# Optimization experiments

Hardware: AMD Instinct MI355X
Metric: run time of the kernel (lower is better)

The kernel has to match this reference:

```python
import jax, jax.numpy as jnp
import numpy as np

N, E, G = 50000, 800000, 64
IN, H, C = 128, 3, 64
HC = H * C


def _conv(x, src, dst, Wq, bq, Wk, bk, Wv, bv, Ws, bs, Wb):
    # node-level projections, then per-edge gather
    q = (x @ Wq + bq).reshape(-1, H, C)[dst]   # [E,H,C]
    k = (x @ Wk + bk).reshape(-1, H, C)[src]
    v = (x @ Wv + bv).reshape(-1, H, C)[src]
    alpha = (q * k).sum(-1) / jnp.sqrt(jnp.float32(C))  # [E,H]
    # segment softmax over incoming edges of each target node
    amax = jax.ops.segment_max(alpha, dst, num_segments=N)
    amax = jnp.where(jnp.isfinite(amax), amax, 0.0)
    ex = jnp.exp(alpha - amax[dst])
    denom = jax.ops.segment_sum(ex, dst, num_segments=N)
    a = ex / (denom[dst] + 1e-16)
    out = jax.ops.segment_sum(a[:, :, None] * v, dst, num_segments=N).reshape(-1, HC)
    # gated skip (beta=True, root_weight=True)
    r = x @ Ws + bs
    beta = jax.nn.sigmoid(jnp.concatenate([out, r, out - r], -1) @ Wb)  # [N,1]
    return beta * r + (1.0 - beta) * out


def setup_inputs() -> dict:
    key = jax.random.key(0)
    ks = jax.random.split(key, 32)
    x = jax.random.normal(ks[0], (N, IN), dtype=jnp.float32)
    edge_index = jax.random.randint(ks[1], (2, E), 0, N, dtype=jnp.int32)
    batch = jnp.sort(jax.random.randint(ks[2], (N,), 0, G, dtype=jnp.int32))
    s = 0.05
    def w(k, shape):
        return jax.random.normal(k, shape, dtype=jnp.float32) * s
    d = {"x": x, "edge_index": edge_index, "batch": batch}
    ins = [IN, HC]
    ki = 3
    for l in range(2):
        din = ins[l]
        d[f"Wq{l}"] = w(ks[ki], (din, HC)); ki += 1
        d[f"bq{l}"] = jnp.zeros((HC,), jnp.float32)
        d[f"Wk{l}"] = w(ks[ki], (din, HC)); ki += 1
        d[f"bk{l}"] = jnp.zeros((HC,), jnp.float32)
        d[f"Wv{l}"] = w(ks[ki], (din, HC)); ki += 1
        d[f"bv{l}"] = jnp.zeros((HC,), jnp.float32)
        d[f"Ws{l}"] = w(ks[ki], (din, HC)); ki += 1
        d[f"bs{l}"] = jnp.zeros((HC,), jnp.float32)
        d[f"Wb{l}"] = w(ks[ki], (3 * HC, 1)); ki += 1
    d["Wlin"] = w(ks[ki], (HC, 1)); ki += 1
    d["blin"] = jnp.zeros((1,), jnp.float32)
    return d


def reference(x, edge_index, batch,
              Wq0, bq0, Wk0, bk0, Wv0, bv0, Ws0, bs0, Wb0,
              Wq1, bq1, Wk1, bk1, Wv1, bv1, Ws1, bs1, Wb1,
              Wlin, blin):
    src, dst = edge_index[0], edge_index[1]
    h = _conv(x, src, dst, Wq0, bq0, Wk0, bk0, Wv0, bv0, Ws0, bs0, Wb0)
    h = jax.nn.elu(h)
    h = _conv(h, src, dst, Wq1, bq1, Wk1, bk1, Wv1, bv1, Ws1, bs1, Wb1)
    h = jax.nn.elu(h)
    # global mean pool over graphs
    cnt = jax.ops.segment_sum(jnp.ones((N,), jnp.float32), batch, num_segments=G)
    pooled = jax.ops.segment_sum(h, batch, num_segments=G) / jnp.maximum(cnt, 1.0)[:, None]
    logits = (pooled @ Wlin + blin).squeeze(-1)  # [G]
    return logits
```

## Files before the change

### kernel.cpp

```cpp
#include <hip/hip_runtime.h>
#include <math.h>

#define NNODES 50000
#define NEDGES 800000
#define NGRAPH 64
#define DIM_IN 128
#define HCDIM  192
#define QKVRW  768

typedef __attribute__((ext_vector_type(8))) short short8;
typedef __attribute__((ext_vector_type(4))) float f32x4;
typedef __attribute__((ext_vector_type(2))) float f32x2;

__device__ __forceinline__ unsigned short f2bf(float f){
  unsigned int u = __float_as_uint(f);
  unsigned int r = (u + 0x7fffu + ((u>>16)&1u)) >> 16;
  return (unsigned short)r;
}

__device__ __forceinline__ float4 bf4_to_f4(uint2 u){
  float4 f;
  f.x = __uint_as_float(u.x<<16);
  f.y = __uint_as_float(u.x & 0xffff0000u);
  f.z = __uint_as_float(u.y<<16);
  f.w = __uint_as_float(u.y & 0xffff0000u);
  return f;
}

__device__ __forceinline__ float4 fp8x4_to_f4(unsigned int u){
  f32x2 lo = __builtin_amdgcn_cvt_pk_f32_fp8((int)u, false);
  f32x2 hi = __builtin_amdgcn_cvt_pk_f32_fp8((int)u, true);
  float4 f; f.x=lo[0]; f.y=lo[1]; f.z=hi[0]; f.w=hi[1];
  return f;
}

__device__ __forceinline__ float wave_sum(float v){
#pragma unroll
  for(int off=32; off>0; off>>=1) v += __shfl_xor(v, off, 64);
  return v;
}

__global__ void zero2_k(int* a, int* b, int n){
  int i = blockIdx.x*blockDim.x + threadIdx.x;
  if(i<n){ a[i]=0; b[i]=0; }
}

__global__ void hist_k(const int* __restrict__ dst, int* __restrict__ counts, int E){
  int e = blockIdx.x*blockDim.x + threadIdx.x;
  if(e<E) atomicAdd(&counts[dst[e]], 1);
}

__global__ void scan_partial(const int* __restrict__ counts, int* __restrict__ bsum, int N){
  __shared__ int lds[256];
  int t = threadIdx.x;
  int idx = blockIdx.x*256 + t;
  int v = (idx<N)? counts[idx] : 0;
  lds[t]=v; __syncthreads();
#pragma unroll
  for(int off=128; off>0; off>>=1){
    if(t<off) lds[t]+=lds[t+off];
    __syncthreads();
  }
  if(t==0) bsum[blockIdx.x]=lds[0];
}

__global__ void scan_bsum(int* bsum, int nb){
  __shared__ int lds[1024];
  int t=threadIdx.x;
  int v=(t<nb)?bsum[t]:0;
  lds[t]=v; __syncthreads();
  int x=v;
#pragma unroll
  for(int off=1; off<1024; off<<=1){
    int y=(t>=off)?lds[t-off]:0;
    __syncthreads();
    x+=y; lds[t]=x;
    __syncthreads();
  }
  if(t<nb) bsum[t]=x-v;
}

__global__ void scan_final(const int* __restrict__ counts, const int* __restrict__ bsum,
                           int* __restrict__ row_ptr, int N){
  __shared__ int lds[256];
  int t=threadIdx.x;
  int idx=blockIdx.x*256+t;
  int v=(idx<N)?counts[idx]:0;
  lds[t]=v; __syncthreads();
  int x=v;
#pragma unroll
  for(int off=1; off<256; off<<=1){
    int y=(t>=off)?lds[t-off]:0;
    __syncthreads();
    x+=y; lds[t]=x;
    __syncthreads();
  }
  if(idx<=N) row_ptr[idx]= bsum[blockIdx.x]+x-v;
}

__global__ void fill_k(const int* __restrict__ src, const int* __restrict__ dst,
                       const int* __restrict__ row_ptr, int* __restrict__ cursor,
                       int* __restrict__ csr_src, int E){
  int e = blockIdx.x*blockDim.x + threadIdx.x;
  if(e<E){
    int d = dst[e];
    int pos = row_ptr[d] + atomicAdd(&cursor[d], 1);
    csr_src[pos] = src[e];
  }
}

#define CAST_BLKS (NNODES*DIM_IN/4/256)
__global__ void prep0_k(const float* __restrict__ X, unsigned short* __restrict__ Xb,
                        const float* __restrict__ Wq, const float* __restrict__ Wk,
                        const float* __restrict__ Wv, const float* __restrict__ Ws,
                        const float* __restrict__ bq, const float* __restrict__ bk,
                        const float* __restrict__ bv, const float* __restrict__ bs,
                        unsigned short* __restrict__ Wt, float* __restrict__ bcat){
  if(blockIdx.x < CAST_BLKS){
    int i4 = (blockIdx.x*256 + threadIdx.x)*4;
    float4 v = *(const float4*)(X+i4);
    ushort4 o; o.x=f2bf(v.x); o.y=f2bf(v.y); o.z=f2bf(v.z); o.w=f2bf(v.w);
    *(ushort4*)(Xb+i4) = o;
  } else {
    int idx = (blockIdx.x-CAST_BLKS)*256 + threadIdx.x;
    if(idx < QKVRW*DIM_IN){
      int c = idx / DIM_IN, k = idx % DIM_IN;
      int mat = c/HCDIM, cm = c%HCDIM;
      const float* W = (mat==0)?Wq:(mat==1)?Ws:(mat==2)?Wk:Wv;
      Wt[(size_t)c*DIM_IN + k] = f2bf(W[(size_t)k*HCDIM + cm]);
    }
    if(idx < QKVRW){
      int mat = idx/HCDIM, cm = idx%HCDIM;
      const float* b = (mat==0)?bq:(mat==1)?bs:(mat==2)?bk:bv;
      bcat[idx] = b[cm];
    }
  }
}

__global__ void build_wt(const float* __restrict__ Wq, const float* __restrict__ Wk,
                         const float* __restrict__ Wv, const float* __restrict__ Ws,
                         const float* __restrict__ bq, const float* __restrict__ bk,
                         const float* __restrict__ bv, const float* __restrict__ bs,
                         unsigned short* __restrict__ Wt, float* __restrict__ bcat, int K){
  int idx = blockIdx.x*256 + threadIdx.x;
  if(idx < QKVRW*K){
    int c = idx / K, k = idx % K;
    int mat = c/HCDIM, cm = c%HCDIM;
    const float* W = (mat==0)?Wq:(mat==1)?Ws:(mat==2)?Wk:Wv;
    Wt[(size_t)c*K + k] = f2bf(W[(size_t)k*HCDIM + cm]);
  }
  if(idx < QKVRW){
    int mat = idx/HCDIM, cm = idx%HCDIM;
    const float* b = (mat==0)?bq:(mat==1)?bs:(mat==2)?bk:bv;
    bcat[idx] = b[cm];
  }
}

template<int K>
__global__ __launch_bounds__(256) void gemm_mfma(
    const unsigned short* __restrict__ Xb,
    const unsigned short* __restrict__ Wt,
    const float* __restrict__ bcat,
    unsigned short* __restrict__ QR,
    unsigned char* __restrict__ KV, int N)
{
  __shared__ unsigned short As[128*64];
  __shared__ unsigned short Bs[128*64];
  const int tid = threadIdx.x;
  const int wv = tid>>6;
  const int lane = tid&63;
  const int m0  = blockIdx.x*128;
  const int nc0 = blockIdx.y*128;

  const int wr = wv>>1, wc = wv&1;
  const int lhi = lane>>4, llo = lane&15;
  f32x4 acc[4][4] = {};

  constexpr int NT = K/64;
#pragma unroll
  for(int kt=0; kt<NT; ++kt){
    if(kt>0) __syncthreads();
#pragma unroll
    for(int it=0; it<4; ++it){
      int p = it*256 + tid;
      int r = p>>3, c = p&7;
      int cs = c ^ (r&7);
      int grow = m0 + r; if(grow > N-1) grow = N-1;
      const unsigned short* gp = Xb + (size_t)grow*K + kt*64 + cs*8;
      unsigned short* lp = As + (size_t)(it*256 + wv*64)*8;
      __builtin_amdgcn_global_load_lds(
          (const __attribute__((address_space(1))) unsigned int*)gp,
          (__attribute__((address_space(3))) unsigned int*)lp, 16, 0, 0);
    }
#pragma unroll
    for(int it=0; it<4; ++it){
      int p = it*256 + tid;
      int r = p>>3, c = p&7;
      int cs = c ^ (r&7);
      const unsigned short* gp = Wt + (size_t)(nc0 + r)*K + kt*64 + cs*8;
      unsigned short* lp = Bs + (size_t)(it*256 + wv*64)*8;
      __builtin_amdgcn_global_load_lds(
          (const __attribute__((address_space(1))) unsigned int*)gp,
          (__attribute__((address_space(3))) unsigned int*)lp, 16, 0, 0);
    }
    __syncthreads();

#pragma unroll
    for(int kk=0; kk<64; kk+=32){
      short8 a[4], b[4];
      const int chunk = (kk>>3) + lhi;
#pragma unroll
      for(int i=0;i<4;++i){
        int rr = wr*64 + i*16 + llo;
        int cs = chunk ^ (rr&7);
        a[i] = *(const short8*)(As + rr*64 + cs*8);
      }
#pragma unroll
      for(int j=0;j<4;++j){
        int cc = wc*64 + j*16 + llo;
        int cs = chunk ^ (cc&7);
        b[j] = *(const short8*)(Bs + cc*64 + cs*8);
      }
#pragma unroll
      for(int i=0;i<4;++i)
#pragma unroll
        for(int j=0;j<4;++j)
          acc[i][j] = __builtin_amdgcn_mfma_f32_16x16x32_bf16(a[i], b[j], acc[i][j], 0,0,0);
    }
  }

  if(nc0 < 384){
#pragma unroll
    for(int j=0;j<4;++j){
      const int col = nc0 + wc*64 + j*16 + llo;
      const float bias = bcat[col];
#pragma unroll
      for(int i=0;i<4;++i){
#pragma unroll
        for(int r=0;r<4;++r){
          int grow = m0 + wr*64 + i*16 + lhi*4 + r;
          if(grow < N) QR[(size_t)grow*384 + col] = f2bf(acc[i][j][r] + bias);
        }
      }
    }
  } else {
#pragma unroll
    for(int j=0;j<4;++j){
      const int col = nc0 - 384 + wc*64 + j*16 + llo;
      const float bias = bcat[col + 384];
#pragma unroll
      for(int i=0;i<4;++i){
#pragma unroll
        for(int r=0;r<4;++r){
          int grow = m0 + wr*64 + i*16 + lhi*4 + r;
          float v0 = acc[i][j][r] + bias;
          float n0 = __shfl_xor(v0, 1, 64);
          if(((llo&1)==0) && grow < N){
            int p0 = __builtin_amdgcn_cvt_pk_fp8_f32(v0, n0, 0, false);
            *(unsigned short*)(KV + (size_t)grow*384 + col) = (unsigned short)(p0 & 0xffff);
          }
        }
      }
    }
  }
}

template<bool OUTBF>
__global__ __launch_bounds__(256) void attn_kernel(
  const unsigned short* __restrict__ QR,
  const unsigned char* __restrict__ KV,
  const int* __restrict__ row_ptr, const int* __restrict__ csr_src,
  const float* __restrict__ Wb, float* __restrict__ HoutF,
  unsigned short* __restrict__ HoutB, int N)
{
  const int wave = threadIdx.x>>6;
  const int lane = threadIdx.x&63;
  const int g    = lane>>4;
  const int l    = lane&15;
  const int n = blockIdx.x*4 + wave;
  if(n>=N) return;

  const unsigned short* nr = QR + (size_t)n*384 + 4*l;
  float4 q0 = bf4_to_f4(*(const uint2*)(nr));
  float4 q1 = bf4_to_f4(*(const uint2*)(nr+64));
  float4 q2 = bf4_to_f4(*(const uint2*)(nr+128));

  const int s0 = row_ptr[n];
  const int deg = row_ptr[n+1]-s0;

  float4 a0={0,0,0,0}, a1={0,0,0,0}, a2={0,0,0,0};
  float d0=0.f,d1=0.f,d2=0.f;

  unsigned int ku0=0,ku1=0,ku2=0,vu0=0,vu1=0,vu2=0;
  if(deg>0){
    int i0 = s0 + (g<deg ? g : 0); if(i0 > NEDGES-1) i0 = NEDGES-1;
    int sCur = csr_src[i0];
    const unsigned int* kv = (const unsigned int*)(KV + (size_t)sCur*384) + l;
    ku0=kv[0]; ku1=kv[16]; ku2=kv[32]; vu0=kv[48]; vu1=kv[64]; vu2=kv[80];
  }
  for(int base=0; base<deg; base+=4){
    const int inext = base + 4 + g;
    const int sNxt = csr_src[s0 + (inext<deg ? inext : 0)];
    const unsigned int* kvN = (const unsigned int*)(KV + (size_t)sNxt*384) + l;
    unsigned int nk0=kvN[0], nk1=kvN[16], nk2=kvN[32];
    unsigned int nv0=kvN[48], nv1=kvN[64], nv2=kvN[80];

    const bool valid = (base + g < deg);
    float4 k0 = fp8x4_to_f4(ku0);
    float4 k1 = fp8x4_to_f4(ku1);
    float4 k2 = fp8x4_to_f4(ku2);
    float p0 = q0.x*k0.x+q0.y*k0.y+q0.z*k0.z+q0.w*k0.w;
    float p1 = q1.x*k1.x+q1.y*k1.y+q1.z*k1.z+q1.w*k1.w;
    float p2 = q2.x*k2.x+q2.y*k2.y+q2.z*k2.z+q2.w*k2.w;
#pragma unroll
    for(int off=1; off<16; off<<=1){
      p0 += __shfl_xor(p0, off, 64);
      p1 += __shfl_xor(p1, off, 64);
      p2 += __shfl_xor(p2, off, 64);
    }
    float e0 = valid ? __expf(0.125f*p0) : 0.f;
    float e1 = valid ? __expf(0.125f*p1) : 0.f;
    float e2 = valid ? __expf(0.125f*p2) : 0.f;
    d0 += e0; d1 += e1; d2 += e2;
    float4 v0 = fp8x4_to_f4(vu0);
    float4 v1 = fp8x4_to_f4(vu1);
    float4 v2 = fp8x4_to_f4(vu2);
    a0.x+=e0*v0.x; a0.y+=e0*v0.y; a0.z+=e0*v0.z; a0.w+=e0*v0.w;
    a1.x+=e1*v1.x; a1.y+=e1*v1.y; a1.z+=e1*v1.z; a1.w+=e1*v1.w;
    a2.x+=e2*v2.x; a2.y+=e2*v2.y; a2.z+=e2*v2.z; a2.w+=e2*v2.w;

    ku0=nk0; ku1=nk1; ku2=nk2; vu0=nv0; vu1=nv1; vu2=nv2;
  }

#pragma unroll
  for(int off=16; off<64; off<<=1){
    a0.x+=__shfl_xor(a0.x,off,64); a0.y+=__shfl_xor(a0.y,off,64);
    a0.z+=__shfl_xor(a0.z,off,64); a0.w+=__shfl_xor(a0.w,off,64);
    a1.x+=__shfl_xor(a1.x,off,64); a1.y+=__shfl_xor(a1.y,off,64);
    a1.z+=__shfl_xor(a1.z,off,64); a1.w+=__shfl_xor(a1.w,off,64);
    a2.x+=__shfl_xor(a2.x,off,64); a2.y+=__shfl_xor(a2.y,off,64);
    a2.z+=__shfl_xor(a2.z,off,64); a2.w+=__shfl_xor(a2.w,off,64);
    d0+=__shfl_xor(d0,off,64); d1+=__shfl_xor(d1,off,64); d2+=__shfl_xor(d2,off,64);
  }
  const float id0=1.f/(d0+1e-16f), id1=1.f/(d1+1e-16f), id2=1.f/(d2+1e-16f);
  float4 o0, o1, o2;
  o0.x=a0.x*id0; o0.y=a0.y*id0; o0.z=a0.z*id0; o0.w=a0.w*id0;
  o1.x=a1.x*id1; o1.y=a1.y*id1; o1.z=a1.z*id1; o1.w=a1.w*id1;
  o2.x=a2.x*id2; o2.y=a2.y*id2; o2.z=a2.z*id2; o2.w=a2.w*id2;

  float4 r0 = bf4_to_f4(*(const uint2*)(nr+192));
  float4 r1 = bf4_to_f4(*(const uint2*)(nr+256));
  float4 r2 = bf4_to_f4(*(const uint2*)(nr+320));

  const float* wb = Wb + 4*l;
  float4 w00=*(const float4*)(wb),     w01=*(const float4*)(wb+64),  w02=*(const float4*)(wb+128);
  float4 w10=*(const float4*)(wb+192), w11=*(const float4*)(wb+256), w12=*(const float4*)(wb+320);
  float4 w20=*(const float4*)(wb+384), w21=*(const float4*)(wb+448), w22=*(const float4*)(wb+512);
  float z =
    o0.x*w00.x+o0.y*w00.y+o0.z*w00.z+o0.w*w00.w +
    o1.x*w01.x+o1.y*w01.y+o1.z*w01.z+o1.w*w01.w +
    o2.x*w02.x+o2.y*w02.y+o2.z*w02.z+o2.w*w02.w +
    r0.x*w10.x+r0.y*w10.y+r0.z*w10.z+r0.w*w10.w +
    r1.x*w11.x+r1.y*w11.y+r1.z*w11.z+r1.w*w11.w +
    r2.x*w12.x+r2.y*w12.y+r2.z*w12.z+r2.w*w12.w +
    (o0.x-r0.x)*w20.x+(o0.y-r0.y)*w20.y+(o0.z-r0.z)*w20.z+(o0.w-r0.w)*w20.w +
    (o1.x-r1.x)*w21.x+(o1.y-r1.y)*w21.y+(o1.z-r1.z)*w21.z+(o1.w-r1.w)*w21.w +
    (o2.x-r2.x)*w22.x+(o2.y-r2.y)*w22.y+(o2.z-r2.z)*w22.z+(o2.w-r2.w)*w22.w;
#pragma unroll
  for(int off=1; off<16; off<<=1) z += __shfl_xor(z, off, 64);
  const float beta = 1.f/(1.f+__expf(-z));
  float4 h0,h1,h2;
  h0.x=beta*r0.x+(1.f-beta)*o0.x; h0.y=beta*r0.y+(1.f-beta)*o0.y;
  h0.z=beta*r0.z+(1.f-beta)*o0.z; h0.w=beta*r0.w+(1.f-beta)*o0.w;
  h1.x=beta*r1.x+(1.f-beta)*o1.x; h1.y=beta*r1.y+(1.f-beta)*o1.y;
  h1.z=beta*r1.z+(1.f-beta)*o1.z; h1.w=beta*r1.w+(1.f-beta)*o1.w;
  h2.x=beta*r2.x+(1.f-beta)*o2.x; h2.y=beta*r2.y+(1.f-beta)*o2.y;
  h2.z=beta*r2.z+(1.f-beta)*o2.z; h2.w=beta*r2.w+(1.f-beta)*o2.w;
  h0.x=(h0.x>0.f)?h0.x:expm1f(h0.x); h0.y=(h0.y>0.f)?h0.y:expm1f(h0.y);
  h0.z=(h0.z>0.f)?h0.z:expm1f(h0.z); h0.w=(h0.w>0.f)?h0.w:expm1f(h0.w);
  h1.x=(h1.x>0.f)?h1.x:expm1f(h1.x); h1.y=(h1.y>0.f)?h1.y:expm1f(h1.y);
  h1.z=(h1.z>0.f)?h1.z:expm1f(h1.z); h1.w=(h1.w>0.f)?h1.w:expm1f(h1.w);
  h2.x=(h2.x>0.f)?h2.x:expm1f(h2.x); h2.y=(h2.y>0.f)?h2.y:expm1f(h2.y);
  h2.z=(h2.z>0.f)?h2.z:expm1f(h2.z); h2.w=(h2.w>0.f)?h2.w:expm1f(h2.w);
  if(g==0){
    if(OUTBF){
      unsigned short* hb = HoutB + (size_t)n*HCDIM + 4*l;
      ushort4 u0, u1, u2;
      u0.x=f2bf(h0.x); u0.y=f2bf(h0.y); u0.z=f2bf(h0.z); u0.w=f2bf(h0.w);
      u1.x=f2bf(h1.x); u1.y=f2bf(h1.y); u1.z=f2bf(h1.z); u1.w=f2bf(h1.w);
      u2.x=f2bf(h2.x); u2.y=f2bf(h2.y); u2.z=f2bf(h2.z); u2.w=f2bf(h2.w);
      *(ushort4*)(hb)     = u0;
      *(ushort4*)(hb+64)  = u1;
      *(ushort4*)(hb+128) = u2;
    } else {
      float* ho = HoutF + (size_t)n*HCDIM + 4*l;
      *(float4*)(ho)     = h0;
      *(float4*)(ho+64)  = h1;
      *(float4*)(ho+128) = h2;
    }
  }
}

__global__ void zero_pool(float* pooled, int* cnt){
  int i = blockIdx.x*256 + threadIdx.x;
  if(i < NGRAPH*HCDIM) ((int*)pooled)[i]=0;
  if(i < NGRAPH) cnt[i]=0;
}

__global__ void pool_k(const float* __restrict__ H, const int* __restrict__ batch,
                       float* __restrict__ pooled, int* __restrict__ cnt, int N){
  const int t = threadIdx.x;
  int start = blockIdx.x*256;
  int end = min(start+256, N);
  if(start>=N) return;
  int cur = batch[start];
  float acc = 0.f;
  int run = 0;
  for(int nn=start; nn<end; ++nn){
    int g = batch[nn];
    if(g!=cur){
      atomicAdd(&pooled[(size_t)cur*HCDIM+t], acc);
      if(t==0) atomicAdd(&cnt[cur], run);
      acc=0.f; run=0; cur=g;
    }
    acc += H[(size_t)nn*HCDIM+t];
    run++;
  }
  atomicAdd(&pooled[(size_t)cur*HCDIM+t], acc);
  if(t==0) atomicAdd(&cnt[cur], run);
}

__global__ void logits_k(const float* __restrict__ pooled, const int* __restrict__ cnt,
                         const float* __restrict__ Wlin, const float* __restrict__ blin,
                         float* __restrict__ out){
  const int g = blockIdx.x;
  const int lane = threadIdx.x;
  float c = fmaxf((float)cnt[g], 1.f);
  float s = 0.f;
#pragma unroll
  for(int j=0;j<3;++j){
    int col = j*64+lane;
    s += pooled[(size_t)g*HCDIM+col]/c * Wlin[col];
  }
  s = wave_sum(s);
  if(lane==0) out[g] = s + blin[0];
}

extern "C" void kernel_launch(void* const* d_in, const int* in_sizes, int n_in,
                              void* d_out, int out_size, void* d_ws, size_t ws_size,
                              hipStream_t stream)
{
  const int N=NNODES, E=NEDGES;
  const float* x     = (const float*)d_in[0];
  const int*   ei    = (const int*)d_in[1];
  const int*   batch = (const int*)d_in[2];
  const int* esrc = ei;
  const int* edst = ei + E;
  const float* Wq0=(const float*)d_in[3];  const float* bq0=(const float*)d_in[4];
  const float* Wk0=(const float*)d_in[5];  const float* bk0=(const float*)d_in[6];
  const float* Wv0=(const float*)d_in[7];  const float* bv0=(const float*)d_in[8];
  const float* Ws0=(const float*)d_in[9];  const float* bs0=(const float*)d_in[10];
  const float* Wb0=(const float*)d_in[11];
  const float* Wq1=(const float*)d_in[12]; const float* bq1=(const float*)d_in[13];
  const float* Wk1=(const float*)d_in[14]; const float* bk1=(const float*)d_in[15];
  const float* Wv1=(const float*)d_in[16]; const float* bv1=(const float*)d_in[17];
  const float* Ws1=(const float*)d_in[18]; const float* bs1=(const float*)d_in[19];
  const float* Wb1=(const float*)d_in[20];
  const float* Wlin=(const float*)d_in[21];
  const float* blin=(const float*)d_in[22];
  float* out = (float*)d_out;

  char* p = (char*)d_ws;
  auto alloc = [&](size_t bytes)->char*{
    char* q = p; p += (bytes+255)/256*256; return q;
  };
  unsigned short* Xb   = (unsigned short*)alloc((size_t)N*HCDIM*2);
  unsigned short* QR   = (unsigned short*)alloc((size_t)N*384*2);
  unsigned char*  KV   = (unsigned char*)alloc((size_t)N*384);
  float* H1            = (float*)alloc((size_t)N*HCDIM*4);
  unsigned short* Wt   = (unsigned short*)alloc((size_t)QKVRW*HCDIM*2);
  float* bcat          = (float*)alloc(QKVRW*4);
  int* counts  = (int*)alloc((size_t)N*4);
  int* cursor  = (int*)alloc((size_t)N*4);
  int* row_ptr = (int*)alloc((size_t)(N+1)*4);
  int* csr     = (int*)alloc((size_t)E*4);
  int* bsum    = (int*)alloc(4096);
  float* pooled= (float*)alloc((size_t)NGRAPH*HCDIM*4);
  int* cnt     = (int*)alloc(256);

  const int NB = (N+255)/256;

  zero2_k<<<(N+255)/256,256,0,stream>>>(counts,cursor,N);
  hist_k<<<(E+255)/256,256,0,stream>>>(edst,counts,E);
  scan_partial<<<NB,256,0,stream>>>(counts,bsum,N);
  scan_bsum<<<1,1024,0,stream>>>(bsum,NB);
  scan_final<<<NB,256,0,stream>>>(counts,bsum,row_ptr,N);
  fill_k<<<(E+255)/256,256,0,stream>>>(esrc,edst,row_ptr,cursor,csr,E);

  dim3 ggemm((N+127)/128, 6);
  prep0_k<<<CAST_BLKS + (QKVRW*DIM_IN+255)/256, 256, 0, stream>>>(
      x, Xb, Wq0,Wk0,Wv0,Ws0, bq0,bk0,bv0,bs0, Wt, bcat);
  gemm_mfma<DIM_IN><<<ggemm,256,0,stream>>>(Xb,Wt,bcat,QR,KV,N);
  attn_kernel<true><<<(N+3)/4,256,0,stream>>>(QR,KV,row_ptr,csr,Wb0,nullptr,Xb,N);
  build_wt<<<(QKVRW*HCDIM+255)/256,256,0,stream>>>(Wq1,Wk1,Wv1,Ws1,bq1,bk1,bv1,bs1,Wt,bcat,HCDIM);
  gemm_mfma<HCDIM><<<ggemm,256,0,stream>>>(Xb,Wt,bcat,QR,KV,N);
  attn_kernel<false><<<(N+3)/4,256,0,stream>>>(QR,KV,row_ptr,csr,Wb1,H1,nullptr,N);

  zero_pool<<<(NGRAPH*HCDIM+255)/256,256,0,stream>>>(pooled,cnt);
  pool_k<<<(N+255)/256,192,0,stream>>>(H1,batch,pooled,cnt,N);
  logits_k<<<NGRAPH,64,0,stream>>>(pooled,cnt,Wlin,blin,out);
}
```

Baseline: 408.5 us.

## Merge weight prep kernels, use memsets, and pack attention math into float2 ops

Folds the layer-0 and layer-1 weight transpose/cast into one prep kernel with separate weight buffers. The zeroing kernels are replaced by hipMemsetAsync calls, which cuts the launch count. The attention kernel is rewritten around float2 vectors so the compiler can emit packed FMA, and the 1/sqrt(C) scale is folded into q once instead of applied per edge. Operation order changes slightly, which can shift rounding.

```diff
diff --git a/kernel.cpp b/kernel.cpp
--- a/kernel.cpp
+++ b/kernel.cpp
@@ -18,31 +18,24 @@
   return (unsigned short)r;
 }
 
-__device__ __forceinline__ float4 bf4_to_f4(uint2 u){
-  float4 f;
-  f.x = __uint_as_float(u.x<<16);
-  f.y = __uint_as_float(u.x & 0xffff0000u);
-  f.z = __uint_as_float(u.y<<16);
-  f.w = __uint_as_float(u.y & 0xffff0000u);
-  return f;
-}
-
-__device__ __forceinline__ float4 fp8x4_to_f4(unsigned int u){
-  f32x2 lo = __builtin_amdgcn_cvt_pk_f32_fp8((int)u, false);
-  f32x2 hi = __builtin_amdgcn_cvt_pk_f32_fp8((int)u, true);
-  float4 f; f.x=lo[0]; f.y=lo[1]; f.z=hi[0]; f.w=hi[1];
-  return f;
+__device__ __forceinline__ f32x2 bf2_to_f2(unsigned int u){
+  f32x2 r;
+  r[0] = __uint_as_float(u<<16);
+  r[1] = __uint_as_float(u & 0xffff0000u);
+  return r;
+}
+
+__device__ __forceinline__ f32x2 fp8_lo(unsigned int u){
+  return __builtin_amdgcn_cvt_pk_f32_fp8((int)u, false);
+}
+__device__ __forceinline__ f32x2 fp8_hi(unsigned int u){
+  return __builtin_amdgcn_cvt_pk_f32_fp8((int)u, true);
 }
 
 __device__ __forceinline__ float wave_sum(float v){
 #pragma unroll
   for(int off=32; off>0; off>>=1) v += __shfl_xor(v, off, 64);
   return v;
-}
-
-__global__ void zero2_k(int* a, int* b, int n){
-  int i = blockIdx.x*blockDim.x + threadIdx.x;
-  if(i<n){ a[i]=0; b[i]=0; }
 }
 
 __global__ void hist_k(const int* __restrict__ dst, int* __restrict__ counts, int E){
@@ -110,49 +103,52 @@
 }
 
 #define CAST_BLKS (NNODES*DIM_IN/4/256)
-__global__ void prep0_k(const float* __restrict__ X, unsigned short* __restrict__ Xb,
-                        const float* __restrict__ Wq, const float* __restrict__ Wk,
-                        const float* __restrict__ Wv, const float* __restrict__ Ws,
-                        const float* __restrict__ bq, const float* __restrict__ bk,
-                        const float* __restrict__ bv, const float* __restrict__ bs,
-                        unsigned short* __restrict__ Wt, float* __restrict__ bcat){
-  if(blockIdx.x < CAST_BLKS){
-    int i4 = (blockIdx.x*256 + threadIdx.x)*4;
+#define WT0_BLKS  ((QKVRW*DIM_IN+255)/256)
+#define WT1_BLKS  ((QKVRW*HCDIM+255)/256)
+__global__ void prep_all(const float* __restrict__ X, unsigned short* __restrict__ Xb,
+  const float* __restrict__ Wq0,const float* __restrict__ Wk0,
+  const float* __restrict__ Wv0,const float* __restrict__ Ws0,
+  const float* __restrict__ bq0,const float* __restrict__ bk0,
+  const float* __restrict__ bv0,const float* __restrict__ bs0,
+  unsigned short* __restrict__ Wt0, float* __restrict__ bcat0,
+  const float* __restrict__ Wq1,const float* __restrict__ Wk1,
+  const float* __restrict__ Wv1,const float* __restrict__ Ws1,
+  const float* __restrict__ bq1,const float* __restrict__ bk1,
+  const float* __restrict__ bv1,const float* __restrict__ bs1,
+  unsigned short* __restrict__ Wt1, float* __restrict__ bcat1)
+{
+  const int b = blockIdx.x;
+  if(b < CAST_BLKS){
+    int i4 = (b*256 + threadIdx.x)*4;
     float4 v = *(const float4*)(X+i4);
     ushort4 o; o.x=f2bf(v.x); o.y=f2bf(v.y); o.z=f2bf(v.z); o.w=f2bf(v.w);
     *(ushort4*)(Xb+i4) = o;
-  } else {
-    int idx = (blockIdx.x-CAST_BLKS)*256 + threadIdx.x;
+  } else if(b < CAST_BLKS+WT0_BLKS){
+    int idx = (b-CAST_BLKS)*256 + threadIdx.x;
     if(idx < QKVRW*DIM_IN){
       int c = idx / DIM_IN, k = idx % DIM_IN;
       int mat = c/HCDIM, cm = c%HCDIM;
-      const float* W = (mat==0)?Wq:(mat==1)?Ws:(mat==2)?Wk:Wv;
-      Wt[(size_t)c*DIM_IN + k] = f2bf(W[(size_t)k*HCDIM + cm]);
+      const float* W = (mat==0)?Wq0:(mat==1)?Ws0:(mat==2)?Wk0:Wv0;
+      Wt0[(size_t)c*DIM_IN + k] = f2bf(W[(size_t)k*HCDIM + cm]);
     }
     if(idx < QKVRW){
       int mat = idx/HCDIM, cm = idx%HCDIM;
-      const float* b = (mat==0)?bq:(mat==1)?bs:(mat==2)?bk:bv;
-      bcat[idx] = b[cm];
-    }
-  }
-}
-
-__global__ void build_wt(const float* __restrict__ Wq, const float* __restrict__ Wk,
-                         const float* __restrict__ Wv, const float* __restrict__ Ws,
-                         const float* __restrict__ bq, const float* __restrict__ bk,
-                         const float* __restrict__ bv, const float* __restrict__ bs,
-                         unsigned short* __restrict__ Wt, float* __restrict__ bcat, int K){
-  int idx = blockIdx.x*256 + threadIdx.x;
-  if(idx < QKVRW*K){
-    int c = idx / K, k = idx % K;
-    int mat = c/HCDIM, cm = c%HCDIM;
-    const float* W = (mat==0)?Wq:(mat==1)?Ws:(mat==2)?Wk:Wv;
-    Wt[(size_t)c*K + k] = f2bf(W[(size_t)k*HCDIM + cm]);
-  }
-  if(idx < QKVRW){
-    int mat = idx/HCDIM, cm = idx%HCDIM;
-    const float* b = (mat==0)?bq:(mat==1)?bs:(mat==2)?bk:bv;
-    bcat[idx] = b[cm];
+      const float* bb = (mat==0)?bq0:(mat==1)?bs0:(mat==2)?bk0:bv0;
+      bcat0[idx] = bb[cm];
+    }
+  } else {
+    int idx = (b-CAST_BLKS-WT0_BLKS)*256 + threadIdx.x;
+    if(idx < QKVRW*HCDIM){
+      int c = idx / HCDIM, k = idx % HCDIM;
+      int mat = c/HCDIM, cm = c%HCDIM;
+      const float* W = (mat==0)?Wq1:(mat==1)?Ws1:(mat==2)?Wk1:Wv1;
+      Wt1[(size_t)c*HCDIM + k] = f2bf(W[(size_t)k*HCDIM + cm]);
+    }
+    if(idx < QKVRW){
+      int mat = idx/HCDIM, cm = idx%HCDIM;
+      const float* bb = (mat==0)?bq1:(mat==1)?bs1:(mat==2)?bk1:bv1;
+      bcat1[idx] = bb[cm];
+    }
   }
 }
 
@@ -281,14 +277,19 @@
   if(n>=N) return;
 
   const unsigned short* nr = QR + (size_t)n*384 + 4*l;
-  float4 q0 = bf4_to_f4(*(const uint2*)(nr));
-  float4 q1 = bf4_to_f4(*(const uint2*)(nr+64));
-  float4 q2 = bf4_to_f4(*(const uint2*)(nr+128));
+  f32x2 qlo[3], qhi[3];
+#pragma unroll
+  for(int h=0;h<3;++h){
+    uint2 u = *(const uint2*)(nr + 64*h);
+    qlo[h] = bf2_to_f2(u.x) * 0.125f;
+    qhi[h] = bf2_to_f2(u.y) * 0.125f;
+  }
 
   const int s0 = row_ptr[n];
   const int deg = row_ptr[n+1]-s0;
 
-  float4 a0={0,0,0,0}, a1={0,0,0,0}, a2={0,0,0,0};
+  f32x2 aLo[3] = {{0,0},{0,0},{0,0}};
+  f32x2 aHi[3] = {{0,0},{0,0},{0,0}};
   float d0=0.f,d1=0.f,d2=0.f;
 
   unsigned int ku0=0,ku1=0,ku2=0,vu0=0,vu1=0,vu2=0;
@@ -306,105 +307,92 @@
     unsigned int nv0=kvN[48], nv1=kvN[64], nv2=kvN[80];
 
     const bool valid = (base + g < deg);
-    float4 k0 = fp8x4_to_f4(ku0);
-    float4 k1 = fp8x4_to_f4(ku1);
-    float4 k2 = fp8x4_to_f4(ku2);
-    float p0 = q0.x*k0.x+q0.y*k0.y+q0.z*k0.z+q0.w*k0.w;
-    float p1 = q1.x*k1.x+q1.y*k1.y+q1.z*k1.z+q1.w*k1.w;
-    float p2 = q2.x*k2.x+q2.y*k2.y+q2.z*k2.z+q2.w*k2.w;
+    f32x2 t0 = qlo[0]*fp8_lo(ku0) + qhi[0]*fp8_hi(ku0);
+    f32x2 t1 = qlo[1]*fp8_lo(ku1) + qhi[1]*fp8_hi(ku1);
+    f32x2 t2 = qlo[2]*fp8_lo(ku2) + qhi[2]*fp8_hi(ku2);
+    float p0 = t0[0]+t0[1];
+    float p1 = t1[0]+t1[1];
+    float p2 = t2[0]+t2[1];
 #pragma unroll
     for(int off=1; off<16; off<<=1){
       p0 += __shfl_xor(p0, off, 64);
       p1 += __shfl_xor(p1, off, 64);
       p2 += __shfl_xor(p2, off, 64);
     }
-    float e0 = valid ? __expf(0.125f*p0) : 0.f;
-    float e1 = valid ? __expf(0.125f*p1) : 0.f;
-    float e2 = valid ? __expf(0.125f*p2) : 0.f;
+    float e0 = valid ? __expf(p0) : 0.f;
+    float e1 = valid ? __expf(p1) : 0.f;
+    float e2 = valid ? __expf(p2) : 0.f;
     d0 += e0; d1 += e1; d2 += e2;
-    float4 v0 = fp8x4_to_f4(vu0);
-    float4 v1 = fp8x4_to_f4(vu1);
-    float4 v2 = fp8x4_to_f4(vu2);
-    a0.x+=e0*v0.x; a0.y+=e0*v0.y; a0.z+=e0*v0.z; a0.w+=e0*v0.w;
-    a1.x+=e1*v1.x; a1.y+=e1*v1.y; a1.z+=e1*v1.z; a1.w+=e1*v1.w;
-    a2.x+=e2*v2.x; a2.y+=e2*v2.y; a2.z+=e2*v2.z; a2.w+=e2*v2.w;
+    f32x2 e20 = {e0,e0}, e21 = {e1,e1}, e22 = {e2,e2};
+    aLo[0] = fp8_lo(vu0)*e20 + aLo[0];
+    aHi[0] = fp8_hi(vu0)*e20 + aHi[0];
+    aLo[1] = fp8_lo(vu1)*e21 + aLo[1];
+    aHi[1] = fp8_hi(vu1)*e21 + aHi[1];
+    aLo[2] = fp8_lo(vu2)*e22 + aLo[2];
+    aHi[2] = fp8_hi(vu2)*e22 + aHi[2];
 
     ku0=nk0; ku1=nk1; ku2=nk2; vu0=nv0; vu1=nv1; vu2=nv2;
   }
 
 #pragma unroll
   for(int off=16; off<64; off<<=1){
-    a0.x+=__shfl_xor(a0.x,off,64); a0.y+=__shfl_xor(a0.y,off,64);
-    a0.z+=__shfl_xor(a0.z,off,64); a0.w+=__shfl_xor(a0.w,off,64);
-    a1.x+=__shfl_xor(a1.x,off,64); a1.y+=__shfl_xor(a1.y,off,64);
-    a1.z+=__shfl_xor(a1.z,off,64); a1.w+=__shfl_xor(a1.w,off,64);
-    a2.x+=__shfl_xor(a2.x,off,64); a2.y+=__shfl_xor(a2.y,off,64);
-    a2.z+=__shfl_xor(a2.z,off,64); a2.w+=__shfl_xor(a2.w,off,64);
+#pragma unroll
+    for(int h=0;h<3;++h){
+      aLo[h][0]+=__shfl_xor(aLo[h][0],off,64); aLo[h][1]+=__shfl_xor(aLo[h][1],off,64);
+      aHi[h][0]+=__shfl_xor(aHi[h][0],off,64); aHi[h][1]+=__shfl_xor(aHi[h][1],off,64);
+    }
     d0+=__shfl_xor(d0,off,64); d1+=__shfl_xor(d1,off,64); d2+=__shfl_xor(d2,off,64);
   }
-  const float id0=1.f/(d0+1e-16f), id1=1.f/(d1+1e-16f), id2=1.f/(d2+1e-16f);
-  float4 o0, o1, o2;
-  o0.x=a0.x*id0; o0.y=a0.y*id0; o0.z=a0.z*id0; o0.w=a0.w*id0;
-  o1.x=a1.x*id1; o1.y=a1.y*id1; o1.z=a1.z*id1; o1.w=a1.w*id1;
-  o2.x=a2.x*id2; o2.y=a2.y*id2; o2.z=a2.z*id2; o2.w=a2.w*id2;
-
-  float4 r0 = bf4_to_f4(*(const uint2*)(nr+192));
-  float4 r1 = bf4_to_f4(*(const uint2*)(nr+256));
-  float4 r2 = bf4_to_f4(*(const uint2*)(nr+320));
-
-  const float* wb = Wb + 4*l;
-  float4 w00=*(const float4*)(wb),     w01=*(const float4*)(wb+64),  w02=*(const float4*)(wb+128);
-  float4 w10=*(const float4*)(wb+192), w11=*(const float4*)(wb+256), w12=*(const float4*)(wb+320);
-  float4 w20=*(const float4*)(wb+384), w21=*(const float4*)(wb+448), w22=*(const float4*)(wb+512);
-  float z =
-    o0.x*w00.x+o0.y*w00.y+o0.z*w00.z+o0.w*w00.w +
-    o1.x*w01.x+o1.y*w01.y+o1.z*w01.z+o1.w*w01.w +
-    o2.x*w02.x+o2.y*w02.y+o2.z*w02.z+o2.w*w02.w +
-    r0.x*w10.x+r0.y*w10.y+r0.z*w10.z+r0.w*w10.w +
-    r1.x*w11.x+r1.y*w11.y+r1.z*w11.z+r1.w*w11.w +
-    r2.x*w12.x+r2.y*w12.y+r2.z*w12.z+r2.w*w12.w +
-    (o0.x-r0.x)*w20.x+(o0.y-r0.y)*w20.y+(o0.z-r0.z)*w20.z+(o0.w-r0.w)*w20.w +
-    (o1.x-r1.x)*w21.x+(o1.y-r1.y)*w21.y+(o1.z-r1.z)*w21.z+(o1.w-r1.w)*w21.w +
-    (o2.x-r2.x)*w22.x+(o2.y-r2.y)*w22.y+(o2.z-r2.z)*w22.z+(o2.w-r2.w)*w22.w;
+  const float dsum[3] = {d0,d1,d2};
+  f32x2 oLo[3], oHi[3], rLo[3], rHi[3];
+#pragma unroll
+  for(int h=0;h<3;++h){
+    float inv = 1.f/(dsum[h]+1e-16f);
+    oLo[h] = aLo[h]*inv; oHi[h] = aHi[h]*inv;
+    uint2 ur = *(const uint2*)(nr + 192 + 64*h);
+    rLo[h] = bf2_to_f2(ur.x); rHi[h] = bf2_to_f2(ur.y);
+  }
+
+  f32x2 zz = {0,0};
+#pragma unroll
+  for(int h=0;h<3;++h){
+    const float* wO = Wb + 64*h + 4*l;
+    const float* wR = Wb + 192 + 64*h + 4*l;
+    const float* wD = Wb + 384 + 64*h + 4*l;
+    f32x2 woL = *(const f32x2*)(wO), woH = *(const f32x2*)(wO+2);
+    f32x2 wrL = *(const f32x2*)(wR), wrH = *(const f32x2*)(wR+2);
+    f32x2 wdL = *(const f32x2*)(wD), wdH = *(const f32x2*)(wD+2);
+    zz = oLo[h]*woL + zz;
+    zz = oHi[h]*woH + zz;
+    zz = rLo[h]*wrL + zz;
+    zz = rHi[h]*wrH + zz;
+    zz = (oLo[h]-rLo[h])*wdL + zz;
+    zz = (oHi[h]-rHi[h])*wdH + zz;
+  }
+  float z = zz[0]+zz[1];
 #pragma unroll
   for(int off=1; off<16; off<<=1) z += __shfl_xor(z, off, 64);
   const float beta = 1.f/(1.f+__expf(-z));
-  float4 h0,h1,h2;
-  h0.x=beta*r0.x+(1.f-beta)*o0.x; h0.y=beta*r0.y+(1.f-beta)*o0.y;
-  h0.z=beta*r0.z+(1.f-beta)*o0.z; h0.w=beta*r0.w+(1.f-beta)*o0.w;
-  h1.x=beta*r1.x+(1.f-beta)*o1.x; h1.y=beta*r1.y+(1.f-beta)*o1.y;
-  h1.z=beta*r1.z+(1.f-beta)*o1.z; h1.w=beta*r1.w+(1.f-beta)*o1.w;
-  h2.x=beta*r2.x+(1.f-beta)*o2.x; h2.y=beta*r2.y+(1.f-beta)*o2.y;
-  h2.z=beta*r2.z+(1.f-beta)*o2.z; h2.w=beta*r2.w+(1.f-beta)*o2.w;
-  h0.x=(h0.x>0.f)?h0.x:expm1f(h0.x); h0.y=(h0.y>0.f)?h0.y:expm1f(h0.y);
-  h0.z=(h0.z>0.f)?h0.z:expm1f(h0.z); h0.w=(h0.w>0.f)?h0.w:expm1f(h0.w);
-  h1.x=(h1.x>0.f)?h1.x:expm1f(h1.x); h1.y=(h1.y>0.f)?h1.y:expm1f(h1.y);
-  h1.z=(h1.z>0.f)?h1.z:expm1f(h1.z); h1.w=(h1.w>0.f)?h1.w:expm1f(h1.w);
-  h2.x=(h2.x>0.f)?h2.x:expm1f(h2.x); h2.y=(h2.y>0.f)?h2.y:expm1f(h2.y);
-  h2.z=(h2.z>0.f)?h2.z:expm1f(h2.z); h2.w=(h2.w>0.f)?h2.w:expm1f(h2.w);
+
   if(g==0){
-    if(OUTBF){
-      unsigned short* hb = HoutB + (size_t)n*HCDIM + 4*l;
-      ushort4 u0, u1, u2;
-      u0.x=f2bf(h0.x); u0.y=f2bf(h0.y); u0.z=f2bf(h0.z); u0.w=f2bf(h0.w);
-      u1.x=f2bf(h1.x); u1.y=f2bf(h1.y); u1.z=f2bf(h1.z); u1.w=f2bf(h1.w);
-      u2.x=f2bf(h2.x); u2.y=f2bf(h2.y); u2.z=f2bf(h2.z); u2.w=f2bf(h2.w);
-      *(ushort4*)(hb)     = u0;
-      *(ushort4*)(hb+64)  = u1;
-      *(ushort4*)(hb+128) = u2;
-    } else {
-      float* ho = HoutF + (size_t)n*HCDIM + 4*l;
-      *(float4*)(ho)     = h0;
-      *(float4*)(ho+64)  = h1;
-      *(float4*)(ho+128) = h2;
-    }
-  }
-}
-
-__global__ void zero_pool(float* pooled, int* cnt){
-  int i = blockIdx.x*256 + threadIdx.x;
-  if(i < NGRAPH*HCDIM) ((int*)pooled)[i]=0;
-  if(i < NGRAPH) cnt[i]=0;
+#pragma unroll
+    for(int h=0;h<3;++h){
+      f32x2 hL = (rLo[h]-oLo[h])*beta + oLo[h];
+      f32x2 hH = (rHi[h]-oHi[h])*beta + oHi[h];
+      hL[0]=(hL[0]>0.f)?hL[0]:expm1f(hL[0]); hL[1]=(hL[1]>0.f)?hL[1]:expm1f(hL[1]);
+      hH[0]=(hH[0]>0.f)?hH[0]:expm1f(hH[0]); hH[1]=(hH[1]>0.f)?hH[1]:expm1f(hH[1]);
+      if(OUTBF){
+        unsigned short* hb = HoutB + (size_t)n*HCDIM + 64*h + 4*l;
+        ushort4 u;
+        u.x=f2bf(hL[0]); u.y=f2bf(hL[1]); u.z=f2bf(hH[0]); u.w=f2bf(hH[1]);
+        *(ushort4*)(hb) = u;
+      } else {
+        float* ho = HoutF + (size_t)n*HCDIM + 64*h + 4*l;
+        float4 f; f.x=hL[0]; f.y=hL[1]; f.z=hH[0]; f.w=hH[1];
+        *(float4*)(ho) = f;
+      }
+    }
+  }
 }
 
 __global__ void pool_k(const float* __restrict__ H, const int* __restrict__ batch,
@@ -478,10 +466,13 @@
   unsigned short* QR   = (unsigned short*)alloc((size_t)N*384*2);
   unsigned char*  KV   = (unsigned char*)alloc((size_t)N*384);
   float* H1            = (float*)alloc((size_t)N*HCDIM*4);
-  unsigned short* Wt   = (unsigned short*)alloc((size_t)QKVRW*HCDIM*2);
-  float* bcat          = (float*)alloc(QKVRW*4);
-  int* counts  = (int*)alloc((size_t)N*4);
-  int* cursor  = (int*)alloc((size_t)N*4);
+  unsigned short* Wt0  = (unsigned short*)alloc((size_t)QKVRW*DIM_IN*2);
+  float* bcat0         = (float*)alloc(QKVRW*4);
+  unsigned short* Wt1  = (unsigned short*)alloc((size_t)QKVRW*HCDIM*2);
+  float* bcat1         = (float*)alloc(QKVRW*4);
+  const size_t CSR_CHUNK = ((size_t)N*4+255)/256*256;
+  int* counts  = (int*)alloc(CSR_CHUNK);
+  int* cursor  = (int*)alloc(CSR_CHUNK);
   int* row_ptr = (int*)alloc((size_t)(N+1)*4);
   int* csr     = (int*)alloc((size_t)E*4);
   int* bsum    = (int*)alloc(4096);
@@ -490,7 +481,14 @@
 
   const int NB = (N+255)/256;
 
-  zero2_k<<<(N+255)/256,256,0,stream>>>(counts,cursor,N);
+  hipMemsetAsync(counts, 0, 2*CSR_CHUNK, stream);
+  hipMemsetAsync(pooled, 0, (size_t)NGRAPH*HCDIM*4 + 256, stream);
+
+  prep_all<<<CAST_BLKS + WT0_BLKS + WT1_BLKS, 256, 0, stream>>>(
+      x, Xb,
+      Wq0,Wk0,Wv0,Ws0, bq0,bk0,bv0,bs0, Wt0, bcat0,
+      Wq1,Wk1,Wv1,Ws1, bq1,bk1,bv1,bs1, Wt1, bcat1);
+
   hist_k<<<(E+255)/256,256,0,stream>>>(edst,counts,E);
   scan_partial<<<NB,256,0,stream>>>(counts,bsum,N);
   scan_bsum<<<1,1024,0,stream>>>(bsum,NB);
@@ -498,15 +496,11 @@
   fill_k<<<(E+255)/256,256,0,stream>>>(esrc,edst,row_ptr,cursor,csr,E);
 
   dim3 ggemm((N+127)/128, 6);
-  prep0_k<<<CAST_BLKS + (QKVRW*DIM_IN+255)/256, 256, 0, stream>>>(
-      x, Xb, Wq0,Wk0,Wv0,Ws0, bq0,bk0,bv0,bs0, Wt, bcat);
-  gemm_mfma<DIM_IN><<<ggemm,256,0,stream>>>(Xb,Wt,bcat,QR,KV,N);
+  gemm_mfma<DIM_IN><<<ggemm,256,0,stream>>>(Xb,Wt0,bcat0,QR,KV,N);
   attn_kernel<true><<<(N+3)/4,256,0,stream>>>(QR,KV,row_ptr,csr,Wb0,nullptr,Xb,N);
-  build_wt<<<(QKVRW*HCDIM+255)/256,256,0,stream>>>(Wq1,Wk1,Wv1,Ws1,bq1,bk1,bv1,bs1,Wt,bcat,HCDIM);
-  gemm_mfma<HCDIM><<<ggemm,256,0,stream>>>(Xb,Wt,bcat,QR,KV,N);
+  gemm_mfma<HCDIM><<<ggemm,256,0,stream>>>(Xb,Wt1,bcat1,QR,KV,N);
   attn_kernel<false><<<(N+3)/4,256,0,stream>>>(QR,KV,row_ptr,csr,Wb1,H1,nullptr,N);
 
-  zero_pool<<<(NGRAPH*HCDIM+255)/256,256,0,stream>>>(pooled,cnt);
   pool_k<<<(N+255)/256,192,0,stream>>>(H1,batch,pooled,cnt,N);
   logits_k<<<NGRAPH,64,0,stream>>>(pooled,cnt,Wlin,blin,out);
 }
```

Result: no change. 408.9 us (+0.1%).
